# Optimization experiments

Measured on AMD Instinct MI355X. Metric: run time of the kernel, lower is better.

Reference implementation:

```python
import jax, jax.numpy as jnp
import numpy as np

B, Hs, Ws, C = 1, 48, 48, 768
NH = 12
HD = C // NH          # 64
L = Hs * Ws           # 2304
THETA = 10000.0
SCALE = HD ** -0.5
EPS = 1e-5

# relative coord index table: rel_idx[i, j] = i - j + (H - 1), as in _setup_rel_pos
_REL_IDX = jnp.asarray(np.arange(Hs)[:, None] - np.arange(Ws)[None, :] + (Hs - 1))


def _rope_cos_sin():
    """2D axial RoPE angles (compute_axial_cis): [L, HD//2] cos/sin tables."""
    nf = HD // 4
    freqs = 1.0 / (THETA ** (np.arange(0, HD, 4)[:nf].astype(np.float32) / HD))
    t = np.arange(L, dtype=np.float32)
    tx = t % Hs               # x coord cycles fastest (init_t_xy)
    ty = np.floor(t / Hs)
    ang = np.concatenate([np.outer(tx, freqs), np.outer(ty, freqs)], axis=-1)  # [L, HD//2]
    return jnp.asarray(np.cos(ang)), jnp.asarray(np.sin(ang))


def _layernorm(x, w, b):
    mu = x.mean(-1, keepdims=True)
    var = ((x - mu) ** 2).mean(-1, keepdims=True)
    return (x - mu) * jax.lax.rsqrt(var + EPS) * w + b


def _apply_rope(t, cos, sin):
    # t: [B, NH, L, HD]; view as complex pairs (even=real, odd=imag)
    tr = t.reshape(*t.shape[:-1], HD // 2, 2)
    re, im = tr[..., 0], tr[..., 1]
    out = jnp.stack([re * cos - im * sin, re * sin + im * cos], axis=-1)
    return out.reshape(t.shape)


def setup_inputs() -> dict:
    key = jax.random.key(0)
    ks = jax.random.split(key, 8)
    def rn(k, shape, std=0.02):
        return jax.random.normal(k, shape, dtype=jnp.float32) * std
    return {
        "x": jax.random.normal(ks[0], (B, Hs, Ws, C), dtype=jnp.float32),
        "ln1_w": jnp.ones((C,), jnp.float32),
        "ln1_b": jnp.zeros((C,), jnp.float32),
        "qkv_w": rn(ks[1], (3 * C, C)),
        "qkv_b": jnp.zeros((3 * C,), jnp.float32),
        "rel_pos_h": rn(ks[2], (2 * Hs - 1, HD)),
        "rel_pos_w": rn(ks[3], (2 * Ws - 1, HD)),
        "proj_w": rn(ks[4], (C, C)),
        "proj_b": jnp.zeros((C,), jnp.float32),
        "ln2_w": jnp.ones((C,), jnp.float32),
        "ln2_b": jnp.zeros((C,), jnp.float32),
        "fc1_w": rn(ks[5], (4 * C, C)),
        "fc1_b": jnp.zeros((4 * C,), jnp.float32),
        "fc2_w": rn(ks[6], (C, 4 * C)),
        "fc2_b": jnp.zeros((C,), jnp.float32),
    }


def reference(x, ln1_w, ln1_b, qkv_w, qkv_b, rel_pos_h, rel_pos_w, proj_w, proj_b,
              ln2_w, ln2_b, fc1_w, fc1_b, fc2_w, fc2_b):
    shortcut = x
    h = _layernorm(x, ln1_w, ln1_b)                         # [B,H,W,C]
    qkv = h.reshape(B, L, C) @ qkv_w.T + qkv_b              # [B,L,3C]
    qkv = qkv.reshape(B, L, 3, NH, HD).transpose(2, 0, 3, 1, 4)
    q, k, v = qkv[0], qkv[1], qkv[2]                        # [B,NH,L,HD]

    cos, sin = _rope_cos_sin()
    cos, sin = cos[None, None], sin[None, None]
    q = _apply_rope(q, cos, sin)
    k = _apply_rope(k, cos, sin)

    # Decomposed relative-position bias; math-equivalent to concat_rel_pos
    # (q' = [q*rescale, gathered-rel-vecs], k' = [k, one-hots]) followed by SDPA.
    rq = q.reshape(B, NH, Hs, Ws, HD)
    Rh = rel_pos_h[_REL_IDX]                                # [Hs, Hs(kh), HD]
    Rw = rel_pos_w[_REL_IDX]                                # [Ws, Ws(kw), HD]
    bias_h = jnp.einsum('bnhwc,hkc->bnhwk', rq, Rh)         # over key-row
    bias_w = jnp.einsum('bnhwc,wkc->bnhwk', rq, Rw)         # over key-col

    scores = jnp.einsum('bnqc,bnkc->bnqk', q, k) * SCALE    # [B,NH,L,L]
    scores = scores.reshape(B, NH, Hs, Ws, Hs, Ws) + bias_h[..., :, None] + bias_w[..., None, :]
    attn = jax.nn.softmax(scores.reshape(B, NH, L, L), axis=-1)
    out = jnp.einsum('bnqk,bnkc->bnqc', attn, v)            # [B,NH,L,HD]
    out = out.transpose(0, 2, 1, 3).reshape(B, L, C) @ proj_w.T + proj_b

    x = shortcut + out.reshape(B, Hs, Ws, C)
    h = _layernorm(x, ln2_w, ln2_b)
    h = jax.nn.gelu(h @ fc1_w.T + fc1_b, approximate=False)
    x = x + (h @ fc2_w.T + fc2_b)
    return x
```

## Files before the change

kernel.cpp:

```cpp
#include <hip/hip_runtime.h>
#include <math.h>

#define LTOK 2304
#define CDIM 768
#define NHEAD 12
#define HDIM 64
#define HS 48

typedef short s16x8 __attribute__((ext_vector_type(8)));
typedef float f32x4 __attribute__((ext_vector_type(4)));

__device__ __forceinline__ unsigned short f2b(float f) {
  __bf16 b = (__bf16)f;
  return __builtin_bit_cast(unsigned short, b);
}
__device__ __forceinline__ float b2f(unsigned short u) {
  unsigned int x = ((unsigned int)u) << 16;
  return __builtin_bit_cast(float, x);
}

__device__ __forceinline__ void gld_lds16(void* lds, const void* g) {
  __builtin_amdgcn_global_load_lds(
      (const __attribute__((address_space(1))) unsigned int*)g,
      (__attribute__((address_space(3))) unsigned int*)lds, 16, 0, 0);
}

__global__ __launch_bounds__(256) void f2b4_kernel(const float* __restrict__ a0,
                                                   const float* __restrict__ a1,
                                                   const float* __restrict__ a2,
                                                   const float* __restrict__ a3,
                                                   unsigned short* __restrict__ d0,
                                                   unsigned short* __restrict__ d1,
                                                   unsigned short* __restrict__ d2,
                                                   unsigned short* __restrict__ d3) {
  const int v = blockIdx.x * 256 + threadIdx.x;
  const float* src;
  unsigned short* dst;
  int off;
  if (v < 221184)      { src = a0; dst = d0; off = v; }
  else if (v < 294912) { src = a1; dst = d1; off = v - 221184; }
  else if (v < 589824) { src = a2; dst = d2; off = v - 294912; }
  else                 { src = a3; dst = d3; off = v - 589824; }
  const int i = off * 8;
  float4 v0 = *(const float4*)(src + i);
  float4 v1 = *(const float4*)(src + i + 4);
  alignas(16) unsigned short o[8] = {f2b(v0.x), f2b(v0.y), f2b(v0.z), f2b(v0.w),
                                     f2b(v1.x), f2b(v1.y), f2b(v1.z), f2b(v1.w)};
  *(uint4*)(dst + i) = *(const uint4*)o;
}

__global__ __launch_bounds__(256) void ln_kernel(const float* __restrict__ x,
                                                 const float* __restrict__ w,
                                                 const float* __restrict__ b,
                                                 unsigned short* __restrict__ out) {
  const int row = blockIdx.x;
  const int t = threadIdx.x;
  const float* xr = x + (size_t)row * CDIM;
  float v0 = xr[t], v1 = xr[t + 256], v2 = xr[t + 512];
  float s = v0 + v1 + v2;
  float ss = v0 * v0 + v1 * v1 + v2 * v2;
#pragma unroll
  for (int off = 32; off > 0; off >>= 1) {
    s += __shfl_down(s, off, 64);
    ss += __shfl_down(ss, off, 64);
  }
  __shared__ float rs[4], rss[4];
  if ((t & 63) == 0) { rs[t >> 6] = s; rss[t >> 6] = ss; }
  __syncthreads();
  float S = rs[0] + rs[1] + rs[2] + rs[3];
  float SS = rss[0] + rss[1] + rss[2] + rss[3];
  const float inv_c = 1.0f / (float)CDIM;
  float mu = S * inv_c;
  float var = SS * inv_c - mu * mu;
  float inv = rsqrtf(var + 1e-5f);
  unsigned short* orow = out + (size_t)row * CDIM;
  orow[t]       = f2b((v0 - mu) * inv * w[t]       + b[t]);
  orow[t + 256] = f2b((v1 - mu) * inv * w[t + 256] + b[t + 256]);
  orow[t + 512] = f2b((v2 - mu) * inv * w[t + 512] + b[t + 512]);
}

template <bool GELU, bool RES, bool OUTBF>
__global__ __launch_bounds__(256) void mfma_gemm(const unsigned short* __restrict__ A,
                                                 const unsigned short* __restrict__ B,
                                                 const float* __restrict__ bias,
                                                 const float* __restrict__ res,
                                                 void* __restrict__ Cout,
                                                 int M, int N, int K) {
  __shared__ unsigned short As[2 * 4096];
  __shared__ unsigned short Bs[2 * 4096];
  const int t = threadIdx.x;
  const int lane = t & 63;
  const int w = t >> 6;
  const int wm = w >> 1, wn = w & 1;
  const int bm = blockIdx.y * 128, bn = blockIdx.x * 128;

  f32x4 acc[4][4] = {};

  const int c0 = 2 * w, c1 = 2 * w + 1;
  const int srow = lane >> 2;
  const int skof = (lane & 3) * 8;
  const unsigned short* Abase = A + (size_t)bm * K + skof;
  const unsigned short* Bbase = B + (size_t)bn * K + skof;
  const int lr = lane & 15, lk = (lane >> 4) * 8, lg = lane >> 4;
  const int nk = K >> 5;

  gld_lds16(As + c0 * 512, Abase + (size_t)(c0 * 16 + srow) * K);
  gld_lds16(As + c1 * 512, Abase + (size_t)(c1 * 16 + srow) * K);
  gld_lds16(Bs + c0 * 512, Bbase + (size_t)(c0 * 16 + srow) * K);
  gld_lds16(Bs + c1 * 512, Bbase + (size_t)(c1 * 16 + srow) * K);
  __syncthreads();

#pragma unroll 1
  for (int ks = 0; ks < nk; ++ks) {
    const int off = (ks & 1) * 4096;
    if (ks + 1 < nk) {
      const int noff = 4096 - off;
      const int k1 = (ks + 1) * 32;
      gld_lds16(As + noff + c0 * 512, Abase + (size_t)(c0 * 16 + srow) * K + k1);
      gld_lds16(As + noff + c1 * 512, Abase + (size_t)(c1 * 16 + srow) * K + k1);
      gld_lds16(Bs + noff + c0 * 512, Bbase + (size_t)(c0 * 16 + srow) * K + k1);
      gld_lds16(Bs + noff + c1 * 512, Bbase + (size_t)(c1 * 16 + srow) * K + k1);
    }
    s16x8 a[4], b[4];
#pragma unroll
    for (int m = 0; m < 4; ++m)
      a[m] = *(const s16x8*)&As[off + (wm * 64 + m * 16 + lr) * 32 + lk];
#pragma unroll
    for (int n = 0; n < 4; ++n)
      b[n] = *(const s16x8*)&Bs[off + (wn * 64 + n * 16 + lr) * 32 + lk];
    __builtin_amdgcn_s_setprio(1);
#pragma unroll
    for (int m = 0; m < 4; ++m)
#pragma unroll
      for (int n = 0; n < 4; ++n)
        acc[m][n] = __builtin_amdgcn_mfma_f32_16x16x32_bf16(a[m], b[n], acc[m][n], 0, 0, 0);
    __builtin_amdgcn_s_setprio(0);
    __syncthreads();
  }

#pragma unroll
  for (int n = 0; n < 4; ++n) {
    const int col = bn + wn * 64 + n * 16 + lr;
    const float bc = bias[col];
#pragma unroll
    for (int m = 0; m < 4; ++m) {
#pragma unroll
      for (int j = 0; j < 4; ++j) {
        const int row = bm + wm * 64 + m * 16 + lg * 4 + j;
        float v = acc[m][n][j] + bc;
        if (GELU) v = 0.5f * v * (1.0f + erff(v * 0.70710678118654752f));
        if (RES) v += res[(size_t)row * N + col];
        if (OUTBF) ((unsigned short*)Cout)[(size_t)row * N + col] = f2b(v);
        else       ((float*)Cout)[(size_t)row * N + col] = v;
      }
    }
  }
}

template <bool GELU, bool RES, bool OUTBF>
__global__ __launch_bounds__(256) void gemm64(const unsigned short* __restrict__ A,
                                              const unsigned short* __restrict__ B,
                                              const float* __restrict__ bias,
                                              const float* __restrict__ res,
                                              void* __restrict__ Cout,
                                              int M, int N, int K) {
  __shared__ unsigned short As[2 * 2048];
  __shared__ unsigned short Bs[2 * 4096];
  const int t = threadIdx.x;
  const int lane = t & 63;
  const int w = t >> 6;
  const int wm = w >> 1, wn = w & 1;
  const int bm = blockIdx.y * 64, bn = blockIdx.x * 128;

  f32x4 acc[2][4] = {};

  const int srow = lane >> 2;
  const int skof = (lane & 3) * 8;
  const unsigned short* Abase = A + (size_t)bm * K + skof;
  const unsigned short* Bbase = B + (size_t)bn * K + skof;
  const int lr = lane & 15, lk = (lane >> 4) * 8, lg = lane >> 4;
  const int nk = K >> 5;

  gld_lds16(As + w * 512, Abase + (size_t)(w * 16 + srow) * K);
  gld_lds16(Bs + w * 512, Bbase + (size_t)(w * 16 + srow) * K);
  gld_lds16(Bs + (4 + w) * 512, Bbase + (size_t)((4 + w) * 16 + srow) * K);
  __syncthreads();

#pragma unroll 1
  for (int ks = 0; ks < nk; ++ks) {
    const int offA = (ks & 1) * 2048;
    const int offB = (ks & 1) * 4096;
    if (ks + 1 < nk) {
      const int nA = 2048 - offA, nB = 4096 - offB;
      const int k1 = (ks + 1) * 32;
      gld_lds16(As + nA + w * 512, Abase + (size_t)(w * 16 + srow) * K + k1);
      gld_lds16(Bs + nB + w * 512, Bbase + (size_t)(w * 16 + srow) * K + k1);
      gld_lds16(Bs + nB + (4 + w) * 512, Bbase + (size_t)((4 + w) * 16 + srow) * K + k1);
    }
    s16x8 a[2], b[4];
#pragma unroll
    for (int m = 0; m < 2; ++m)
      a[m] = *(const s16x8*)&As[offA + (wm * 32 + m * 16 + lr) * 32 + lk];
#pragma unroll
    for (int n = 0; n < 4; ++n)
      b[n] = *(const s16x8*)&Bs[offB + (wn * 64 + n * 16 + lr) * 32 + lk];
    __builtin_amdgcn_s_setprio(1);
#pragma unroll
    for (int m = 0; m < 2; ++m)
#pragma unroll
      for (int n = 0; n < 4; ++n)
        acc[m][n] = __builtin_amdgcn_mfma_f32_16x16x32_bf16(a[m], b[n], acc[m][n], 0, 0, 0);
    __builtin_amdgcn_s_setprio(0);
    __syncthreads();
  }

#pragma unroll
  for (int n = 0; n < 4; ++n) {
    const int col = bn + wn * 64 + n * 16 + lr;
    const float bc = bias[col];
#pragma unroll
    for (int m = 0; m < 2; ++m) {
#pragma unroll
      for (int j = 0; j < 4; ++j) {
        const int row = bm + wm * 32 + m * 16 + lg * 4 + j;
        float v = acc[m][n][j] + bc;
        if (GELU) v = 0.5f * v * (1.0f + erff(v * 0.70710678118654752f));
        if (RES) v += res[(size_t)row * N + col];
        if (OUTBF) ((unsigned short*)Cout)[(size_t)row * N + col] = f2b(v);
        else       ((float*)Cout)[(size_t)row * N + col] = v;
      }
    }
  }
}

__global__ __launch_bounds__(256) void rope_cs_kernel(float* __restrict__ cs,
                                                      float* __restrict__ sn) {
  const int idx = blockIdx.x * 256 + threadIdx.x;
  const int l = idx >> 5;
  const int i = idx & 31;
  const int j = i & 15;
  const float f = __expf(-(float)j * 0.57564627324851142f);
  const float coord = (i < 16) ? (float)(l % HS) : (float)(l / HS);
  const float ang = coord * f;
  cs[idx] = cosf(ang);
  sn[idx] = sinf(ang);
}

__global__ __launch_bounds__(256) void prep_kernel(const float* __restrict__ qkv,
                                                   const float* __restrict__ cs,
                                                   const float* __restrict__ sn,
                                                   unsigned short* __restrict__ Qb,
                                                   unsigned short* __restrict__ Kb,
                                                   unsigned short* __restrict__ Vb) {
  __shared__ unsigned short Vs[64 * 72];
  const int t = threadIdx.x;
  const int l0 = blockIdx.x * 64, n = blockIdx.y;
  const int r = t >> 2, c = t & 3;
  const int l = l0 + r;
  const float* base = qkv + (size_t)l * (3 * CDIM) + n * HDIM + c * 16;
#pragma unroll
  for (int pq = 0; pq < 2; ++pq) {
    const float* src = base + pq * CDIM;
    const float qs = pq ? 1.0f : 0.125f;
    alignas(16) unsigned short o[16];
#pragma unroll
    for (int i = 0; i < 4; ++i) {
      float4 v = *(const float4*)(src + i * 4);
      const int pr = c * 8 + i * 2;
      const float c0 = cs[l * 32 + pr],     s0 = sn[l * 32 + pr];
      const float c1 = cs[l * 32 + pr + 1], s1 = sn[l * 32 + pr + 1];
      o[i * 4 + 0] = f2b((v.x * c0 - v.y * s0) * qs);
      o[i * 4 + 1] = f2b((v.x * s0 + v.y * c0) * qs);
      o[i * 4 + 2] = f2b((v.z * c1 - v.w * s1) * qs);
      o[i * 4 + 3] = f2b((v.z * s1 + v.w * c1) * qs);
    }
    unsigned short* dst = (pq ? Kb : Qb) + ((size_t)n * LTOK + l) * HDIM + c * 16;
    *(uint4*)dst = *(const uint4*)o;
    *(uint4*)(dst + 8) = *(const uint4*)(o + 8);
  }
  {
    const float* vsrc = base + 2 * CDIM;
    alignas(16) unsigned short vo[16];
#pragma unroll
    for (int i = 0; i < 4; ++i) {
      float4 v = *(const float4*)(vsrc + i * 4);
      vo[i * 4 + 0] = f2b(v.x); vo[i * 4 + 1] = f2b(v.y);
      vo[i * 4 + 2] = f2b(v.z); vo[i * 4 + 3] = f2b(v.w);
    }
    *(uint4*)&Vs[r * 72 + c * 16] = *(const uint4*)vo;
    *(uint4*)&Vs[r * 72 + c * 16 + 8] = *(const uint4*)(vo + 8);
  }
  __syncthreads();
  {
    const int d = t >> 2, kc16 = (t & 3) * 16;
    alignas(16) unsigned short o[16];
#pragma unroll
    for (int i = 0; i < 16; ++i) o[i] = Vs[(kc16 + i) * 72 + d];
    const int kb = (l0 + kc16) >> 3;
    unsigned short* dst0 = Vb + ((size_t)(n * (LTOK / 8) + kb) * 64 + d) * 8;
    unsigned short* dst1 = Vb + ((size_t)(n * (LTOK / 8) + kb + 1) * 64 + d) * 8;
    *(uint4*)dst0 = *(const uint4*)o;
    *(uint4*)dst1 = *(const uint4*)(o + 8);
  }
}

__global__ __launch_bounds__(256) void attn_mfma(const unsigned short* __restrict__ Qb,
                                                 const unsigned short* __restrict__ Kb,
                                                 const unsigned short* __restrict__ Vb,
                                                 const float* __restrict__ relh,
                                                 const float* __restrict__ relw,
                                                 unsigned short* __restrict__ out) {
  __shared__ __align__(16) unsigned char smem[74752];
  unsigned short* const K_lds = (unsigned short*)(smem);
  unsigned short* const V_lds = (unsigned short*)(smem + 24576);
  unsigned short* const P_lds = (unsigned short*)(smem + 53248);
  float* const bh_t = (float*)(smem + 62464);
  unsigned short* const Q_s = (unsigned short*)(smem + 53248);

  const int t = threadIdx.x;
  const int lane = t & 63, w = t >> 6;
  const int p = lane & 15, g = lane >> 4;
  const int l0 = blockIdx.x * 64, n = blockIdx.y;

  const unsigned short* Khead = Kb + (size_t)n * LTOK * HDIM;
  const unsigned short* Vhead = Vb + (size_t)n * (LTOK / 8) * 64 * 8;

  {
    const int r = t >> 2, c = t & 3;
    const unsigned short* src = Qb + ((size_t)n * LTOK + l0 + r) * HDIM + c * 16;
    uint4 v0 = *(const uint4*)src;
    uint4 v1 = *(const uint4*)(src + 8);
    *(uint4*)&Q_s[r * 72 + c * 16] = v0;
    *(uint4*)&Q_s[r * 72 + c * 16 + 8] = v1;
  }
  __syncthreads();

  const int rowb = lane >> 3;
  const int srcc = (lane & 7) ^ rowb;
  const int kc0 = w, kc1 = w + 4, kc2 = w + 8;

  {
    gld_lds16(K_lds + kc0 * 512, Khead + (size_t)(kc0 * 8 + rowb) * HDIM + srcc * 8);
    gld_lds16(K_lds + kc1 * 512, Khead + (size_t)(kc1 * 8 + rowb) * HDIM + srcc * 8);
    gld_lds16(K_lds + kc2 * 512, Khead + (size_t)(kc2 * 8 + rowb) * HDIM + srcc * 8);
    gld_lds16(V_lds + kc0 * 512, Vhead + kc0 * 512 + lane * 8);
    gld_lds16(V_lds + kc1 * 512, Vhead + kc1 * 512 + lane * 8);
    gld_lds16(V_lds + kc2 * 512, Vhead + kc2 * 512 + lane * 8);
  }
  if (t < 128) *(uint4*)&V_lds[6144 + t * 8] = uint4{0u, 0u, 0u, 0u};
  else         *(uint4*)&V_lds[7168 + 6144 + (t - 128) * 8] = uint4{0u, 0u, 0u, 0u};

  const s16x8 qf0 = *(const s16x8*)&Q_s[(w * 16 + p) * 72 + g * 8];
  const s16x8 qf1 = *(const s16x8*)&Q_s[(w * 16 + p) * 72 + 32 + g * 8];

  const int qh_lane = (l0 + lane) / 48;
#pragma unroll
  for (int i = 0; i < 12; ++i) {
    const int kh = w + 4 * i;
    const float* rrow = relh + (size_t)(qh_lane - kh + 47) * HDIM;
    float acc = 0.f;
#pragma unroll
    for (int c8 = 0; c8 < 8; ++c8) {
      s16x8 qv = *(const s16x8*)&Q_s[lane * 72 + c8 * 8];
      float4 ra = *(const float4*)&rrow[c8 * 8];
      float4 rb = *(const float4*)&rrow[c8 * 8 + 4];
      acc += b2f((unsigned short)qv[0]) * ra.x + b2f((unsigned short)qv[1]) * ra.y +
             b2f((unsigned short)qv[2]) * ra.z + b2f((unsigned short)qv[3]) * ra.w +
             b2f((unsigned short)qv[4]) * rb.x + b2f((unsigned short)qv[5]) * rb.y +
             b2f((unsigned short)qv[6]) * rb.z + b2f((unsigned short)qv[7]) * rb.w;
    }
    bh_t[kh * 64 + lane] = acc * 8.0f;
  }

  float bwreg[12];
  {
    const int qrow = w * 16 + p;
    const int qw_lane = (l0 + qrow) % 48;
#pragma unroll
    for (int mb = 0; mb < 3; ++mb)
#pragma unroll
      for (int jj = 0; jj < 4; ++jj) {
        const int j = 16 * mb + 4 * g + jj;
        const float* rrow = relw + (size_t)(qw_lane - j + 47) * HDIM;
        float acc = 0.f;
#pragma unroll
        for (int c8 = 0; c8 < 8; ++c8) {
          s16x8 qv = *(const s16x8*)&Q_s[qrow * 72 + c8 * 8];
          float4 ra = *(const float4*)&rrow[c8 * 8];
          float4 rb = *(const float4*)&rrow[c8 * 8 + 4];
          acc += b2f((unsigned short)qv[0]) * ra.x + b2f((unsigned short)qv[1]) * ra.y +
                 b2f((unsigned short)qv[2]) * ra.z + b2f((unsigned short)qv[3]) * ra.w +
                 b2f((unsigned short)qv[4]) * rb.x + b2f((unsigned short)qv[5]) * rb.y +
                 b2f((unsigned short)qv[6]) * rb.z + b2f((unsigned short)qv[7]) * rb.w;
        }
        bwreg[mb * 4 + jj] = acc * 8.0f;
      }
  }
  __syncthreads();

  {
    uint2 z = {0u, 0u};
    *(uint2*)&P_lds[(w * 16 + p) * 72 + 48 + 4 * g] = z;
  }

  float lsum = 0.f;
  f32x4 accO[4] = {};
  const int sw0 = g ^ (p & 7);
  const int sw1 = (g + 4) ^ (p & 7);
  unsigned short* const Pw = P_lds + w * 16 * 72;

#pragma unroll 1
  for (int kt = 0; kt < 24; ++kt) {
    const int ko = (kt & 1) * 6144;
    const int vo = (kt & 1) * 7168;
    if (kt < 23) {
      const int nko = 6144 - ko, nvo = 7168 - vo;
      const int kb = (kt + 1) * 96;
      const int vb = (kt + 1) * 12;
      gld_lds16(K_lds + nko + kc0 * 512, Khead + (size_t)(kb + kc0 * 8 + rowb) * HDIM + srcc * 8);
      gld_lds16(K_lds + nko + kc1 * 512, Khead + (size_t)(kb + kc1 * 8 + rowb) * HDIM + srcc * 8);
      gld_lds16(K_lds + nko + kc2 * 512, Khead + (size_t)(kb + kc2 * 8 + rowb) * HDIM + srcc * 8);
      gld_lds16(V_lds + nvo + kc0 * 512, Vhead + (vb + kc0) * 512 + lane * 8);
      gld_lds16(V_lds + nvo + kc1 * 512, Vhead + (vb + kc1) * 512 + lane * 8);
      gld_lds16(V_lds + nvo + kc2 * 512, Vhead + (vb + kc2) * 512 + lane * 8);
    }

#pragma unroll 1
    for (int h = 0; h < 2; ++h) {
      f32x4 st[3] = {};
      __builtin_amdgcn_s_setprio(1);
#pragma unroll
      for (int mb = 0; mb < 3; ++mb) {
        const int krow = ko + (h * 48 + 16 * mb + p) * 64;
        s16x8 kf0 = *(const s16x8*)&K_lds[krow + sw0 * 8];
        s16x8 kf1 = *(const s16x8*)&K_lds[krow + sw1 * 8];
        st[mb] = __builtin_amdgcn_mfma_f32_16x16x32_bf16(kf0, qf0, st[mb], 0, 0, 0);
        st[mb] = __builtin_amdgcn_mfma_f32_16x16x32_bf16(kf1, qf1, st[mb], 0, 0, 0);
      }
      __builtin_amdgcn_s_setprio(0);

      const float bhv = bh_t[(2 * kt + h) * 64 + w * 16 + p] - 8.0f;
      float pv[12], ps = 0.f;
#pragma unroll
      for (int mb = 0; mb < 3; ++mb)
#pragma unroll
        for (int jj = 0; jj < 4; ++jj) {
          const float sv = st[mb][jj] + bhv + bwreg[mb * 4 + jj];
          pv[mb * 4 + jj] = __expf(sv);
          ps += pv[mb * 4 + jj];
        }
      lsum += ps;

#pragma unroll
      for (int mb = 0; mb < 3; ++mb) {
        unsigned int lo = (unsigned int)f2b(pv[mb * 4 + 0]) | ((unsigned int)f2b(pv[mb * 4 + 1]) << 16);
        unsigned int hi = (unsigned int)f2b(pv[mb * 4 + 2]) | ((unsigned int)f2b(pv[mb * 4 + 3]) << 16);
        uint2 val = {lo, hi};
        *(uint2*)&Pw[p * 72 + 16 * mb + 4 * g] = val;
      }

      const s16x8 pf0 = *(const s16x8*)&Pw[p * 72 + g * 8];
      const s16x8 pf1 = *(const s16x8*)&Pw[p * 72 + 32 + g * 8];
      __builtin_amdgcn_s_setprio(1);
#pragma unroll
      for (int db = 0; db < 4; ++db) {
        const int drow = 16 * db + p;
        s16x8 vf0 = *(const s16x8*)&V_lds[vo + ((6 * h + g) * 64 + drow) * 8];
        s16x8 vf1 = *(const s16x8*)&V_lds[vo + ((6 * h + 4 + g) * 64 + drow) * 8];
        accO[db] = __builtin_amdgcn_mfma_f32_16x16x32_bf16(vf0, pf0, accO[db], 0, 0, 0);
        accO[db] = __builtin_amdgcn_mfma_f32_16x16x32_bf16(vf1, pf1, accO[db], 0, 0, 0);
      }
      __builtin_amdgcn_s_setprio(0);
    }

    __syncthreads();
  }

  float ls = lsum + __shfl_xor(lsum, 16, 64);
  ls += __shfl_xor(ls, 32, 64);
  const float inv = 1.0f / ls;
  unsigned short* orow = out + (size_t)(l0 + w * 16 + p) * CDIM + n * HDIM;
#pragma unroll
  for (int db = 0; db < 4; ++db) {
    unsigned int lo = (unsigned int)f2b(accO[db][0] * inv) | ((unsigned int)f2b(accO[db][1] * inv) << 16);
    unsigned int hi = (unsigned int)f2b(accO[db][2] * inv) | ((unsigned int)f2b(accO[db][3] * inv) << 16);
    uint2 val = {lo, hi};
    *(uint2*)&orow[16 * db + 4 * g] = val;
  }
}

extern "C" void kernel_launch(void* const* d_in, const int* in_sizes, int n_in,
                              void* d_out, int out_size, void* d_ws, size_t ws_size,
                              hipStream_t stream) {
  const float* x     = (const float*)d_in[0];
  const float* ln1w  = (const float*)d_in[1];
  const float* ln1b  = (const float*)d_in[2];
  const float* qkvw  = (const float*)d_in[3];
  const float* qkvb  = (const float*)d_in[4];
  const float* relh  = (const float*)d_in[5];
  const float* relw  = (const float*)d_in[6];
  const float* projw = (const float*)d_in[7];
  const float* projb = (const float*)d_in[8];
  const float* ln2w  = (const float*)d_in[9];
  const float* ln2b  = (const float*)d_in[10];
  const float* fc1w  = (const float*)d_in[11];
  const float* fc1b  = (const float*)d_in[12];
  const float* fc2w  = (const float*)d_in[13];
  const float* fc2b  = (const float*)d_in[14];
  float* out = (float*)d_out;
  float* ws = (float*)d_ws;

  float* qkv = ws;
  float* x1  = qkv + (size_t)LTOK * 3 * CDIM;
  float* cs  = x1 + (size_t)LTOK * CDIM;
  float* sn  = cs + (size_t)LTOK * 32;
  unsigned short* h_bf    = (unsigned short*)(sn + (size_t)LTOK * 32);
  unsigned short* attn_bf = h_bf + (size_t)LTOK * CDIM;
  unsigned short* wq      = attn_bf + (size_t)LTOK * CDIM;
  unsigned short* wproj   = wq + (size_t)3 * CDIM * CDIM;
  unsigned short* wfc1    = wproj + (size_t)CDIM * CDIM;
  unsigned short* wfc2    = wfc1 + (size_t)4 * CDIM * CDIM;
  unsigned short* Qb      = (unsigned short*)x1;
  unsigned short* Kb      = Qb + (size_t)NHEAD * LTOK * HDIM;
  unsigned short* Vb      = wq;
  unsigned short* m1_bf   = (unsigned short*)qkv;

  f2b4_kernel<<<3456, 256, 0, stream>>>(qkvw, projw, fc1w, fc2w, wq, wproj, wfc1, wfc2);

  ln_kernel<<<LTOK, 256, 0, stream>>>(x, ln1w, ln1b, h_bf);
  mfma_gemm<false, false, false><<<dim3(18, 18), 256, 0, stream>>>(
      h_bf, wq, qkvb, nullptr, qkv, LTOK, 3 * CDIM, CDIM);
  rope_cs_kernel<<<288, 256, 0, stream>>>(cs, sn);
  prep_kernel<<<dim3(36, 12), 256, 0, stream>>>(qkv, cs, sn, Qb, Kb, Vb);
  attn_mfma<<<dim3(36, 12), 256, 0, stream>>>(Qb, Kb, Vb, relh, relw, attn_bf);
  gemm64<false, true, false><<<dim3(6, 36), 256, 0, stream>>>(
      attn_bf, wproj, projb, x, x1, LTOK, CDIM, CDIM);
  ln_kernel<<<LTOK, 256, 0, stream>>>(x1, ln2w, ln2b, h_bf);
  mfma_gemm<true, false, true><<<dim3(24, 18), 256, 0, stream>>>(
      h_bf, wfc1, fc1b, nullptr, m1_bf, LTOK, 4 * CDIM, CDIM);
  gemm64<false, true, false><<<dim3(6, 36), 256, 0, stream>>>(
      m1_bf, wfc2, fc2b, x1, out, LTOK, CDIM, 4 * CDIM);
}
```

Baseline: 235.9 us.

## Halve attention K/V tile, shrink LDS, store row bias in bf16, swizzle block order

The attention kernel now processes 48 keys per step instead of 96, so the K/V double buffers shrink and total shared memory drops from about 73KB to about 43KB. The row-bias table is stored as bf16 instead of fp32 to fit the smaller layout. This is meant to let more blocks reside per CU to hide latency. A 1D grid with an XCD-style block swizzle groups tiles of the same head, which should improve L2 reuse of that head's K/V. In exchange it doubles the number of loop iterations and __syncthreads barriers, and the bf16 row bias adds rounding error.

New measurement: 239.4 us. About the same (+1.5%).

```diff
diff --git a/kernel.cpp b/kernel.cpp
--- a/kernel.cpp
+++ b/kernel.cpp
@@ -300,7 +300,7 @@
     unsigned short* dst0 = Vb + ((size_t)(n * (LTOK / 8) + kb) * 64 + d) * 8;
     unsigned short* dst1 = Vb + ((size_t)(n * (LTOK / 8) + kb + 1) * 64 + d) * 8;
     *(uint4*)dst0 = *(const uint4*)o;
-    *(uint4*)dst1 = *(const uint4*)(o + 8);
+    *(uint4*)(dst1) = *(const uint4*)(o + 8);
   }
 }
 
@@ -310,17 +310,19 @@
                                                  const float* __restrict__ relh,
                                                  const float* __restrict__ relw,
                                                  unsigned short* __restrict__ out) {
-  __shared__ __align__(16) unsigned char smem[74752];
+  __shared__ __align__(16) unsigned char smem[44032];
   unsigned short* const K_lds = (unsigned short*)(smem);
-  unsigned short* const V_lds = (unsigned short*)(smem + 24576);
-  unsigned short* const P_lds = (unsigned short*)(smem + 53248);
-  float* const bh_t = (float*)(smem + 62464);
-  unsigned short* const Q_s = (unsigned short*)(smem + 53248);
+  unsigned short* const V_lds = (unsigned short*)(smem + 12288);
+  unsigned short* const P_lds = (unsigned short*)(smem + 28672);
+  unsigned short* const bh16 = (unsigned short*)(smem + 37888);
+  unsigned short* const Q_s = (unsigned short*)(smem + 28672);
 
   const int t = threadIdx.x;
   const int lane = t & 63, w = t >> 6;
   const int p = lane & 15, g = lane >> 4;
-  const int l0 = blockIdx.x * 64, n = blockIdx.y;
+  const int bid = blockIdx.x;
+  const int swz = (bid & 7) * 54 + (bid >> 3);
+  const int l0 = (swz % 36) * 64, n = swz / 36;
 
   const unsigned short* Khead = Kb + (size_t)n * LTOK * HDIM;
   const unsigned short* Vhead = Vb + (size_t)n * (LTOK / 8) * 64 * 8;
@@ -337,18 +339,19 @@
 
   const int rowb = lane >> 3;
   const int srcc = (lane & 7) ^ rowb;
-  const int kc0 = w, kc1 = w + 4, kc2 = w + 8;
-
-  {
-    gld_lds16(K_lds + kc0 * 512, Khead + (size_t)(kc0 * 8 + rowb) * HDIM + srcc * 8);
-    gld_lds16(K_lds + kc1 * 512, Khead + (size_t)(kc1 * 8 + rowb) * HDIM + srcc * 8);
-    gld_lds16(K_lds + kc2 * 512, Khead + (size_t)(kc2 * 8 + rowb) * HDIM + srcc * 8);
-    gld_lds16(V_lds + kc0 * 512, Vhead + kc0 * 512 + lane * 8);
-    gld_lds16(V_lds + kc1 * 512, Vhead + kc1 * 512 + lane * 8);
-    gld_lds16(V_lds + kc2 * 512, Vhead + kc2 * 512 + lane * 8);
-  }
-  if (t < 128) *(uint4*)&V_lds[6144 + t * 8] = uint4{0u, 0u, 0u, 0u};
-  else         *(uint4*)&V_lds[7168 + 6144 + (t - 128) * 8] = uint4{0u, 0u, 0u, 0u};
+
+  {
+    gld_lds16(K_lds + w * 512, Khead + (size_t)(w * 8 + rowb) * HDIM + srcc * 8);
+    if (w < 2)
+      gld_lds16(K_lds + (4 + w) * 512, Khead + (size_t)((4 + w) * 8 + rowb) * HDIM + srcc * 8);
+    gld_lds16(V_lds + w * 512, Vhead + w * 512 + lane * 8);
+    if (w >= 2)
+      gld_lds16(V_lds + (2 + w) * 512, Vhead + (2 + w) * 512 + lane * 8);
+  }
+  {
+    const int b = t >> 7;
+    *(uint4*)&V_lds[b * 4096 + 6 * 512 + (t & 127) * 8] = uint4{0u, 0u, 0u, 0u};
+  }
 
   const s16x8 qf0 = *(const s16x8*)&Q_s[(w * 16 + p) * 72 + g * 8];
   const s16x8 qf1 = *(const s16x8*)&Q_s[(w * 16 + p) * 72 + 32 + g * 8];
@@ -369,7 +372,7 @@
              b2f((unsigned short)qv[4]) * rb.x + b2f((unsigned short)qv[5]) * rb.y +
              b2f((unsigned short)qv[6]) * rb.z + b2f((unsigned short)qv[7]) * rb.w;
     }
-    bh_t[kh * 64 + lane] = acc * 8.0f;
+    bh16[kh * 64 + lane] = f2b(acc * 8.0f);
   }
 
   float bwreg[12];
@@ -410,68 +413,66 @@
   unsigned short* const Pw = P_lds + w * 16 * 72;
 
 #pragma unroll 1
-  for (int kt = 0; kt < 24; ++kt) {
-    const int ko = (kt & 1) * 6144;
-    const int vo = (kt & 1) * 7168;
-    if (kt < 23) {
-      const int nko = 6144 - ko, nvo = 7168 - vo;
-      const int kb = (kt + 1) * 96;
-      const int vb = (kt + 1) * 12;
-      gld_lds16(K_lds + nko + kc0 * 512, Khead + (size_t)(kb + kc0 * 8 + rowb) * HDIM + srcc * 8);
-      gld_lds16(K_lds + nko + kc1 * 512, Khead + (size_t)(kb + kc1 * 8 + rowb) * HDIM + srcc * 8);
-      gld_lds16(K_lds + nko + kc2 * 512, Khead + (size_t)(kb + kc2 * 8 + rowb) * HDIM + srcc * 8);
-      gld_lds16(V_lds + nvo + kc0 * 512, Vhead + (vb + kc0) * 512 + lane * 8);
-      gld_lds16(V_lds + nvo + kc1 * 512, Vhead + (vb + kc1) * 512 + lane * 8);
-      gld_lds16(V_lds + nvo + kc2 * 512, Vhead + (vb + kc2) * 512 + lane * 8);
-    }
-
-#pragma unroll 1
-    for (int h = 0; h < 2; ++h) {
-      f32x4 st[3] = {};
-      __builtin_amdgcn_s_setprio(1);
-#pragma unroll
-      for (int mb = 0; mb < 3; ++mb) {
-        const int krow = ko + (h * 48 + 16 * mb + p) * 64;
-        s16x8 kf0 = *(const s16x8*)&K_lds[krow + sw0 * 8];
-        s16x8 kf1 = *(const s16x8*)&K_lds[krow + sw1 * 8];
-        st[mb] = __builtin_amdgcn_mfma_f32_16x16x32_bf16(kf0, qf0, st[mb], 0, 0, 0);
-        st[mb] = __builtin_amdgcn_mfma_f32_16x16x32_bf16(kf1, qf1, st[mb], 0, 0, 0);
+  for (int kt = 0; kt < 48; ++kt) {
+    const int ko = (kt & 1) * 3072;
+    const int vo = (kt & 1) * 4096;
+    if (kt < 47) {
+      const int nko = 3072 - ko, nvo = 4096 - vo;
+      const int kb = (kt + 1) * 48;
+      const int vb = (kt + 1) * 6;
+      gld_lds16(K_lds + nko + w * 512, Khead + (size_t)(kb + w * 8 + rowb) * HDIM + srcc * 8);
+      if (w < 2)
+        gld_lds16(K_lds + nko + (4 + w) * 512,
+                  Khead + (size_t)(kb + (4 + w) * 8 + rowb) * HDIM + srcc * 8);
+      gld_lds16(V_lds + nvo + w * 512, Vhead + (vb + w) * 512 + lane * 8);
+      if (w >= 2)
+        gld_lds16(V_lds + nvo + (2 + w) * 512, Vhead + (vb + 2 + w) * 512 + lane * 8);
+    }
+
+    f32x4 st[3] = {};
+    __builtin_amdgcn_s_setprio(1);
+#pragma unroll
+    for (int mb = 0; mb < 3; ++mb) {
+      const int krow = ko + (16 * mb + p) * 64;
+      s16x8 kf0 = *(const s16x8*)&K_lds[krow + sw0 * 8];
+      s16x8 kf1 = *(const s16x8*)&K_lds[krow + sw1 * 8];
+      st[mb] = __builtin_amdgcn_mfma_f32_16x16x32_bf16(kf0, qf0, st[mb], 0, 0, 0);
+      st[mb] = __builtin_amdgcn_mfma_f32_16x16x32_bf16(kf1, qf1, st[mb], 0, 0, 0);
+    }
+    __builtin_amdgcn_s_setprio(0);
+
+    const float bhv = b2f(bh16[kt * 64 + w * 16 + p]) - 8.0f;
+    float pv[12], ps = 0.f;
+#pragma unroll
+    for (int mb = 0; mb < 3; ++mb)
+#pragma unroll
+      for (int jj = 0; jj < 4; ++jj) {
+        const float sv = st[mb][jj] + bhv + bwreg[mb * 4 + jj];
+        pv[mb * 4 + jj] = __expf(sv);
+        ps += pv[mb * 4 + jj];
       }
-      __builtin_amdgcn_s_setprio(0);
-
-      const float bhv = bh_t[(2 * kt + h) * 64 + w * 16 + p] - 8.0f;
-      float pv[12], ps = 0.f;
-#pragma unroll
-      for (int mb = 0; mb < 3; ++mb)
-#pragma unroll
-        for (int jj = 0; jj < 4; ++jj) {
-          const float sv = st[mb][jj] + bhv + bwreg[mb * 4 + jj];
-          pv[mb * 4 + jj] = __expf(sv);
-          ps += pv[mb * 4 + jj];
-        }
-      lsum += ps;
-
-#pragma unroll
-      for (int mb = 0; mb < 3; ++mb) {
-        unsigned int lo = (unsigned int)f2b(pv[mb * 4 + 0]) | ((unsigned int)f2b(pv[mb * 4 + 1]) << 16);
-        unsigned int hi = (unsigned int)f2b(pv[mb * 4 + 2]) | ((unsigned int)f2b(pv[mb * 4 + 3]) << 16);
-        uint2 val = {lo, hi};
-        *(uint2*)&Pw[p * 72 + 16 * mb + 4 * g] = val;
-      }
-
-      const s16x8 pf0 = *(const s16x8*)&Pw[p * 72 + g * 8];
-      const s16x8 pf1 = *(const s16x8*)&Pw[p * 72 + 32 + g * 8];
-      __builtin_amdgcn_s_setprio(1);
-#pragma unroll
-      for (int db = 0; db < 4; ++db) {
-        const int drow = 16 * db + p;
-        s16x8 vf0 = *(const s16x8*)&V_lds[vo + ((6 * h + g) * 64 + drow) * 8];
-        s16x8 vf1 = *(const s16x8*)&V_lds[vo + ((6 * h + 4 + g) * 64 + drow) * 8];
-        accO[db] = __builtin_amdgcn_mfma_f32_16x16x32_bf16(vf0, pf0, accO[db], 0, 0, 0);
-        accO[db] = __builtin_amdgcn_mfma_f32_16x16x32_bf16(vf1, pf1, accO[db], 0, 0, 0);
-      }
-      __builtin_amdgcn_s_setprio(0);
-    }
+    lsum += ps;
+
+#pragma unroll
+    for (int mb = 0; mb < 3; ++mb) {
+      unsigned int lo = (unsigned int)f2b(pv[mb * 4 + 0]) | ((unsigned int)f2b(pv[mb * 4 + 1]) << 16);
+      unsigned int hi = (unsigned int)f2b(pv[mb * 4 + 2]) | ((unsigned int)f2b(pv[mb * 4 + 3]) << 16);
+      uint2 val = {lo, hi};
+      *(uint2*)&Pw[p * 72 + 16 * mb + 4 * g] = val;
+    }
+
+    const s16x8 pf0 = *(const s16x8*)&Pw[p * 72 + g * 8];
+    const s16x8 pf1 = *(const s16x8*)&Pw[p * 72 + 32 + g * 8];
+    __builtin_amdgcn_s_setprio(1);
+#pragma unroll
+    for (int db = 0; db < 4; ++db) {
+      const int drow = 16 * db + p;
+      s16x8 vf0 = *(const s16x8*)&V_lds[vo + (g * 64 + drow) * 8];
+      s16x8 vf1 = *(const s16x8*)&V_lds[vo + ((4 + g) * 64 + drow) * 8];
+      accO[db] = __builtin_amdgcn_mfma_f32_16x16x32_bf16(vf0, pf0, accO[db], 0, 0, 0);
+      accO[db] = __builtin_amdgcn_mfma_f32_16x16x32_bf16(vf1, pf1, accO[db], 0, 0, 0);
+    }
+    __builtin_amdgcn_s_setprio(0);
 
     __syncthreads();
   }
@@ -532,7 +533,7 @@
       h_bf, wq, qkvb, nullptr, qkv, LTOK, 3 * CDIM, CDIM);
   rope_cs_kernel<<<288, 256, 0, stream>>>(cs, sn);
   prep_kernel<<<dim3(36, 12), 256, 0, stream>>>(qkv, cs, sn, Qb, Kb, Vb);
-  attn_mfma<<<dim3(36, 12), 256, 0, stream>>>(Qb, Kb, Vb, relh, relw, attn_bf);
+  attn_mfma<<<432, 256, 0, stream>>>(Qb, Kb, Vb, relh, relw, attn_bf);
   gemm64<false, true, false><<<dim3(6, 36), 256, 0, stream>>>(
       attn_bf, wproj, projb, x, x1, LTOK, CDIM, CDIM);
   ln_kernel<<<LTOK, 256, 0, stream>>>(x1, ln2w, ln2b, h_bf);
```

## Fuse RoPE, Q scaling and QKV relayout into QKV GEMM epilogue; swizzle attention blocks

Applied to the files above, without the earlier changes.

Adds a dedicated QKV GEMM whose epilogue adds bias, applies RoPE via lane shuffles, scales Q, and writes bf16 Q/K plus a blocked V layout directly. This removes the fp32 qkv intermediate round trip and the separate prep kernel launch. Attention blocks are launched on a 1D grid with a swizzle that spreads heads across XCDs for better L2 locality. V gets its own workspace slot instead of aliasing the QKV weights, and the epilogue now does scattered 2-byte stores.

After: 241.8 us. 1.02x slower.

```diff
diff --git a/kernel.cpp b/kernel.cpp
--- a/kernel.cpp
+++ b/kernel.cpp
@@ -157,6 +157,101 @@
   }
 }
 
+__global__ __launch_bounds__(256) void qkv_gemm(const unsigned short* __restrict__ A,
+                                                const unsigned short* __restrict__ B,
+                                                const float* __restrict__ bias,
+                                                const float* __restrict__ cs,
+                                                const float* __restrict__ sn,
+                                                unsigned short* __restrict__ Qb,
+                                                unsigned short* __restrict__ Kb,
+                                                unsigned short* __restrict__ Vb) {
+  const int K = CDIM;
+  __shared__ unsigned short As[2 * 4096];
+  __shared__ unsigned short Bs[2 * 4096];
+  const int t = threadIdx.x;
+  const int lane = t & 63;
+  const int w = t >> 6;
+  const int wm = w >> 1, wn = w & 1;
+  const int bm = blockIdx.y * 128, bn = blockIdx.x * 128;
+
+  f32x4 acc[4][4] = {};
+
+  const int c0 = 2 * w, c1 = 2 * w + 1;
+  const int srow = lane >> 2;
+  const int skof = (lane & 3) * 8;
+  const unsigned short* Abase = A + (size_t)bm * K + skof;
+  const unsigned short* Bbase = B + (size_t)bn * K + skof;
+  const int lr = lane & 15, lk = (lane >> 4) * 8, lg = lane >> 4;
+  const int nk = K >> 5;
+
+  gld_lds16(As + c0 * 512, Abase + (size_t)(c0 * 16 + srow) * K);
+  gld_lds16(As + c1 * 512, Abase + (size_t)(c1 * 16 + srow) * K);
+  gld_lds16(Bs + c0 * 512, Bbase + (size_t)(c0 * 16 + srow) * K);
+  gld_lds16(Bs + c1 * 512, Bbase + (size_t)(c1 * 16 + srow) * K);
+  __syncthreads();
+
+#pragma unroll 1
+  for (int ks = 0; ks < nk; ++ks) {
+    const int off = (ks & 1) * 4096;
+    if (ks + 1 < nk) {
+      const int noff = 4096 - off;
+      const int k1 = (ks + 1) * 32;
+      gld_lds16(As + noff + c0 * 512, Abase + (size_t)(c0 * 16 + srow) * K + k1);
+      gld_lds16(As + noff + c1 * 512, Abase + (size_t)(c1 * 16 + srow) * K + k1);
+      gld_lds16(Bs + noff + c0 * 512, Bbase + (size_t)(c0 * 16 + srow) * K + k1);
+      gld_lds16(Bs + noff + c1 * 512, Bbase + (size_t)(c1 * 16 + srow) * K + k1);
+    }
+    s16x8 a[4], b[4];
+#pragma unroll
+    for (int m = 0; m < 4; ++m)
+      a[m] = *(const s16x8*)&As[off + (wm * 64 + m * 16 + lr) * 32 + lk];
+#pragma unroll
+    for (int n = 0; n < 4; ++n)
+      b[n] = *(const s16x8*)&Bs[off + (wn * 64 + n * 16 + lr) * 32 + lk];
+    __builtin_amdgcn_s_setprio(1);
+#pragma unroll
+    for (int m = 0; m < 4; ++m)
+#pragma unroll
+      for (int n = 0; n < 4; ++n)
+        acc[m][n] = __builtin_amdgcn_mfma_f32_16x16x32_bf16(a[m], b[n], acc[m][n], 0, 0, 0);
+    __builtin_amdgcn_s_setprio(0);
+    __syncthreads();
+  }
+
+  const int region = bn / CDIM;
+  const int hbase = (bn % CDIM) >> 6;
+#pragma unroll
+  for (int n = 0; n < 4; ++n) {
+    const int cl = wn * 64 + n * 16 + lr;
+    const int col = bn + cl;
+    const int head = hbase + (cl >> 6);
+    const int d = col & 63;
+    const float bc = bias[col];
+#pragma unroll
+    for (int m = 0; m < 4; ++m) {
+#pragma unroll
+      for (int j = 0; j < 4; ++j) {
+        const int row = bm + wm * 64 + m * 16 + lg * 4 + j;
+        const float v = acc[m][n][j] + bc;
+        const float u = __shfl_xor(v, 1, 64);
+        if (region < 2) {
+          const int pi = d >> 1;
+          const float c = cs[row * 32 + pi];
+          const float s = sn[row * 32 + pi];
+          float o = (d & 1) ? (u * s + v * c) : (v * c - u * s);
+          if (region == 0) {
+            Qb[((size_t)head * LTOK + row) * HDIM + d] = f2b(o * 0.125f);
+          } else {
+            Kb[((size_t)head * LTOK + row) * HDIM + d] = f2b(o);
+          }
+        } else {
+          Vb[(((size_t)head * (LTOK / 8) + (row >> 3)) * HDIM + d) * 8 + (row & 7)] = f2b(v);
+        }
+      }
+    }
+  }
+}
+
 template <bool GELU, bool RES, bool OUTBF>
 __global__ __launch_bounds__(256) void gemm64(const unsigned short* __restrict__ A,
                                               const unsigned short* __restrict__ B,
@@ -246,64 +341,6 @@
   sn[idx] = sinf(ang);
 }
 
-__global__ __launch_bounds__(256) void prep_kernel(const float* __restrict__ qkv,
-                                                   const float* __restrict__ cs,
-                                                   const float* __restrict__ sn,
-                                                   unsigned short* __restrict__ Qb,
-                                                   unsigned short* __restrict__ Kb,
-                                                   unsigned short* __restrict__ Vb) {
-  __shared__ unsigned short Vs[64 * 72];
-  const int t = threadIdx.x;
-  const int l0 = blockIdx.x * 64, n = blockIdx.y;
-  const int r = t >> 2, c = t & 3;
-  const int l = l0 + r;
-  const float* base = qkv + (size_t)l * (3 * CDIM) + n * HDIM + c * 16;
-#pragma unroll
-  for (int pq = 0; pq < 2; ++pq) {
-    const float* src = base + pq * CDIM;
-    const float qs = pq ? 1.0f : 0.125f;
-    alignas(16) unsigned short o[16];
-#pragma unroll
-    for (int i = 0; i < 4; ++i) {
-      float4 v = *(const float4*)(src + i * 4);
-      const int pr = c * 8 + i * 2;
-      const float c0 = cs[l * 32 + pr],     s0 = sn[l * 32 + pr];
-      const float c1 = cs[l * 32 + pr + 1], s1 = sn[l * 32 + pr + 1];
-      o[i * 4 + 0] = f2b((v.x * c0 - v.y * s0) * qs);
-      o[i * 4 + 1] = f2b((v.x * s0 + v.y * c0) * qs);
-      o[i * 4 + 2] = f2b((v.z * c1 - v.w * s1) * qs);
-      o[i * 4 + 3] = f2b((v.z * s1 + v.w * c1) * qs);
-    }
-    unsigned short* dst = (pq ? Kb : Qb) + ((size_t)n * LTOK + l) * HDIM + c * 16;
-    *(uint4*)dst = *(const uint4*)o;
-    *(uint4*)(dst + 8) = *(const uint4*)(o + 8);
-  }
-  {
-    const float* vsrc = base + 2 * CDIM;
-    alignas(16) unsigned short vo[16];
-#pragma unroll
-    for (int i = 0; i < 4; ++i) {
-      float4 v = *(const float4*)(vsrc + i * 4);
-      vo[i * 4 + 0] = f2b(v.x); vo[i * 4 + 1] = f2b(v.y);
-      vo[i * 4 + 2] = f2b(v.z); vo[i * 4 + 3] = f2b(v.w);
-    }
-    *(uint4*)&Vs[r * 72 + c * 16] = *(const uint4*)vo;
-    *(uint4*)&Vs[r * 72 + c * 16 + 8] = *(const uint4*)(vo + 8);
-  }
-  __syncthreads();
-  {
-    const int d = t >> 2, kc16 = (t & 3) * 16;
-    alignas(16) unsigned short o[16];
-#pragma unroll
-    for (int i = 0; i < 16; ++i) o[i] = Vs[(kc16 + i) * 72 + d];
-    const int kb = (l0 + kc16) >> 3;
-    unsigned short* dst0 = Vb + ((size_t)(n * (LTOK / 8) + kb) * 64 + d) * 8;
-    unsigned short* dst1 = Vb + ((size_t)(n * (LTOK / 8) + kb + 1) * 64 + d) * 8;
-    *(uint4*)dst0 = *(const uint4*)o;
-    *(uint4*)dst1 = *(const uint4*)(o + 8);
-  }
-}
-
 __global__ __launch_bounds__(256) void attn_mfma(const unsigned short* __restrict__ Qb,
                                                  const unsigned short* __restrict__ Kb,
                                                  const unsigned short* __restrict__ Vb,
@@ -320,7 +357,9 @@
   const int t = threadIdx.x;
   const int lane = t & 63, w = t >> 6;
   const int p = lane & 15, g = lane >> 4;
-  const int l0 = blockIdx.x * 64, n = blockIdx.y;
+  const int bid = blockIdx.x;
+  const int swz = (bid & 7) * 54 + (bid >> 3);
+  const int l0 = (swz % 36) * 64, n = swz / 36;
 
   const unsigned short* Khead = Kb + (size_t)n * LTOK * HDIM;
   const unsigned short* Vhead = Vb + (size_t)n * (LTOK / 8) * 64 * 8;
@@ -520,19 +559,17 @@
   unsigned short* wproj   = wq + (size_t)3 * CDIM * CDIM;
   unsigned short* wfc1    = wproj + (size_t)CDIM * CDIM;
   unsigned short* wfc2    = wfc1 + (size_t)4 * CDIM * CDIM;
+  unsigned short* Vb      = wfc2 + (size_t)4 * CDIM * CDIM;
   unsigned short* Qb      = (unsigned short*)x1;
   unsigned short* Kb      = Qb + (size_t)NHEAD * LTOK * HDIM;
-  unsigned short* Vb      = wq;
   unsigned short* m1_bf   = (unsigned short*)qkv;
 
   f2b4_kernel<<<3456, 256, 0, stream>>>(qkvw, projw, fc1w, fc2w, wq, wproj, wfc1, wfc2);
 
   ln_kernel<<<LTOK, 256, 0, stream>>>(x, ln1w, ln1b, h_bf);
-  mfma_gemm<false, false, false><<<dim3(18, 18), 256, 0, stream>>>(
-      h_bf, wq, qkvb, nullptr, qkv, LTOK, 3 * CDIM, CDIM);
   rope_cs_kernel<<<288, 256, 0, stream>>>(cs, sn);
-  prep_kernel<<<dim3(36, 12), 256, 0, stream>>>(qkv, cs, sn, Qb, Kb, Vb);
-  attn_mfma<<<dim3(36, 12), 256, 0, stream>>>(Qb, Kb, Vb, relh, relw, attn_bf);
+  qkv_gemm<<<dim3(18, 18), 256, 0, stream>>>(h_bf, wq, qkvb, cs, sn, Qb, Kb, Vb);
+  attn_mfma<<<432, 256, 0, stream>>>(Qb, Kb, Vb, relh, relw, attn_bf);
   gemm64<false, true, false><<<dim3(6, 36), 256, 0, stream>>>(
       attn_bf, wproj, projb, x, x1, LTOK, CDIM, CDIM);
   ln_kernel<<<LTOK, 256, 0, stream>>>(x1, ln2w, ln2b, h_bf);
```
